# Performance work log

Measured on AMD Instinct MI355X. Metric: run time of the kernel, lower is better.

## Reference

```python
import jax, jax.numpy as jnp
import numpy as np

N_NODES = 100000
N_EDGES = 1600000
N_FEATS = 128
N_CLASSES = 40
K_HOPS = 3


def setup_inputs() -> dict:
    key = jax.random.key(0)
    k1, k2, k3, k4 = jax.random.split(key, 4)
    x = jax.random.normal(k1, (N_NODES, N_FEATS), dtype=jnp.float32)
    edge_index = jax.random.randint(k2, (2, N_EDGES), 0, N_NODES, dtype=jnp.int64)
    edge_weight = jax.random.uniform(k3, (N_EDGES,), dtype=jnp.float32)
    # Linear layer of SGConv (bias=False): [num_feats, num_classes]
    W = jax.random.normal(k4, (N_FEATS, N_CLASSES), dtype=jnp.float32) / np.sqrt(N_FEATS)
    return {"x": x, "edge_index": edge_index, "edge_weight": edge_weight, "W": W}


def reference(x, edge_index, edge_weight, W):
    # SGConv forward: gcn_norm (symmetric, no self-loops), K hops of
    # edge-weighted gather/scatter aggregation, then linear (lin_first=False).
    row, col = edge_index[0], edge_index[1]
    # symmetric normalization: deg from target-node scatter of edge weights
    deg = jax.ops.segment_sum(edge_weight, col, num_segments=N_NODES)
    deg_inv_sqrt = jnp.where(deg > 0, jax.lax.rsqrt(jnp.maximum(deg, 1e-30)), 0.0)
    norm = deg_inv_sqrt[row] * edge_weight * deg_inv_sqrt[col]  # [E]
    h = x
    for _ in range(K_HOPS):
        msgs = h[row] * norm[:, None]                 # [E, F] gather + scale
        h = jax.ops.segment_sum(msgs, col, num_segments=N_NODES)  # [N, F] scatter-add
    return h @ W  # [N, num_classes]
```

## Files before the change

### kernel.cpp

```cpp
#include <hip/hip_runtime.h>
#include <hip/hip_fp16.h>

namespace {
constexpr int NN = 100000;
constexpr int NE = 1600000;
constexpr int NF = 128;
constexpr int NC = 40;
constexpr int HP = 64;
constexpr int NB = (NN + 255) / 256;
constexpr int EB = (NE + 255) / 256;
constexpr float FIX = 1048576.0f;
constexpr int NPB = 51;
constexpr int HB  = (NN + NPB - 1) / NPB;
constexpr int TS  = 2048;
}

struct alignas(16) H8 { __half2 a, b, c, d; };

__device__ inline __half2 f2h2(float x, float y) {
    return __halves2half2(__float2half_rn(x), __float2half_rn(y));
}

__global__ __launch_bounds__(256, 2) void k_build(const int* __restrict__ col,
                                                  const float* __restrict__ w,
                                                  const float* __restrict__ x,
                                                  const float* __restrict__ W,
                                                  unsigned long long* __restrict__ dc,
                                                  unsigned char* __restrict__ rank,
                                                  __half* __restrict__ h0) {
    if (blockIdx.x < (unsigned)NB) {
        int n = blockIdx.x * 256 + threadIdx.x;
        if (n >= NN) return;
        const float4* xr = (const float4*)(x + (size_t)n * NF);
        const float4* W4 = (const float4*)W;
        float acc[NC];
#pragma unroll
        for (int j = 0; j < NC; ++j) acc[j] = 0.f;
        for (int k4 = 0; k4 < NF / 4; ++k4) {
            float4 xv = xr[k4];
#pragma unroll
            for (int kk = 0; kk < 4; ++kk) {
                float xk = (kk == 0) ? xv.x : (kk == 1) ? xv.y : (kk == 2) ? xv.z : xv.w;
                int k = k4 * 4 + kk;
#pragma unroll
                for (int j4 = 0; j4 < 10; ++j4) {
                    float4 wv = W4[k * 10 + j4];
                    acc[j4 * 4 + 0] += xk * wv.x;
                    acc[j4 * 4 + 1] += xk * wv.y;
                    acc[j4 * 4 + 2] += xk * wv.z;
                    acc[j4 * 4 + 3] += xk * wv.w;
                }
            }
        }
        H8* o = (H8*)(h0 + (size_t)n * HP);
#pragma unroll
        for (int g = 0; g < 5; ++g) {
            H8 v;
            v.a = f2h2(acc[g * 8 + 0], acc[g * 8 + 1]);
            v.b = f2h2(acc[g * 8 + 2], acc[g * 8 + 3]);
            v.c = f2h2(acc[g * 8 + 4], acc[g * 8 + 5]);
            v.d = f2h2(acc[g * 8 + 6], acc[g * 8 + 7]);
            o[g] = v;
        }
    } else {
        int e = (blockIdx.x - NB) * 256 + threadIdx.x;
        if (e >= NE) return;
        int c = col[e];
        unsigned long long q = (unsigned long long)(unsigned)(w[e] * FIX + 0.5f);
        unsigned long long old = atomicAdd(&dc[c], (1ull << 40) | q);
        rank[e] = (unsigned char)(old >> 40);
    }
}

__global__ __launch_bounds__(256) void k_scan1(const unsigned long long* __restrict__ dc,
                                               int* __restrict__ offs,
                                               int* __restrict__ bsum,
                                               float* __restrict__ dis) {
    __shared__ int s[256];
    int t = threadIdx.x, i = blockIdx.x * 256 + t;
    unsigned long long p = (i < NN) ? dc[i] : 0ull;
    int v = (int)(p >> 40);
    if (i < NN) {
        float d = (float)(p & ((1ull << 40) - 1)) * (1.0f / FIX);
        dis[i] = (d > 0.f) ? rsqrtf(d) : 0.f;
    }
    s[t] = v;
    __syncthreads();
    for (int off = 1; off < 256; off <<= 1) {
        int add = (t >= off) ? s[t - off] : 0;
        __syncthreads();
        s[t] += add;
        __syncthreads();
    }
    if (i < NN) offs[i] = s[t] - v;
    if (t == 255) bsum[blockIdx.x] = s[255];
}

__global__ __launch_bounds__(512) void k_scan2(int* __restrict__ bsum) {
    __shared__ int s[512];
    int t = threadIdx.x;
    int v = (t < NB) ? bsum[t] : 0;
    s[t] = v;
    __syncthreads();
    for (int off = 1; off < 512; off <<= 1) {
        int add = (t >= off) ? s[t - off] : 0;
        __syncthreads();
        s[t] += add;
        __syncthreads();
    }
    if (t < NB) bsum[t] = s[t] - v;
}

__global__ __launch_bounds__(256) void k_scatter(const int* __restrict__ row,
                                                 const int* __restrict__ col,
                                                 const float* __restrict__ w,
                                                 const float* __restrict__ dis,
                                                 const int* __restrict__ offs,
                                                 const int* __restrict__ bsum,
                                                 const unsigned char* __restrict__ rank,
                                                 int2* __restrict__ pair) {
    int e = blockIdx.x * 256 + threadIdx.x;
    if (e >= NE) return;
    int r = row[e], c = col[e];
    int p = offs[c] + bsum[c >> 8] + rank[e];
    unsigned long long v = (unsigned long long)(unsigned)r |
        ((unsigned long long)(unsigned)__float_as_int(dis[r] * w[e] * dis[c]) << 32);
    __builtin_nontemporal_store(v, (unsigned long long*)(pair + p));
}

template <bool FINAL>
__global__ __launch_bounds__(256) void k_hop(const int* __restrict__ offs,
                                             const int* __restrict__ bsum,
                                             const int2* __restrict__ pair,
                                             const __half* __restrict__ hin,
                                             __half* __restrict__ houth,
                                             float* __restrict__ houtf) {
    __shared__ int2 tile[TS];
    __shared__ int erange[2];
    int t = threadIdx.x;
    int g = t / 5;
    int n = blockIdx.x * NPB + g;
    bool active = (t < NPB * 5) && (n < NN);
    int vo = (t - g * 5) * 8;
    int s0 = 0, s1 = 0;
    if (active) {
        s0 = offs[n] + bsum[n >> 8];
        int np = n + 1;
        s1 = (np == NN) ? NE : (offs[np] + bsum[np >> 8]);
    }
    if (t == 0) {
        int n0 = blockIdx.x * NPB;
        erange[0] = offs[n0] + bsum[n0 >> 8];
        int nl = n0 + NPB;
        erange[1] = (nl >= NN) ? NE : (offs[nl] + bsum[nl >> 8]);
    }
    __syncthreads();
    int E0 = erange[0], E1 = erange[1];
    float acc[8];
#pragma unroll
    for (int j = 0; j < 8; ++j) acc[j] = 0.f;
    int i = s0;
    for (int t0 = E0; t0 < E1; t0 += TS) {
        int lim = min(t0 + TS, E1);
        int cnt = lim - t0;
        for (int j = t; j < cnt; j += 256) tile[j] = pair[t0 + j];
        __syncthreads();
        if (active) {
            int hi = min(s1, lim);
            for (; i + 2 <= hi; i += 2) {
                int2 p0 = tile[i - t0];
                int2 p1 = tile[i + 1 - t0];
                H8 m0 = *(const H8*)(hin + (size_t)p0.x * HP + vo);
                H8 m1 = *(const H8*)(hin + (size_t)p1.x * HP + vo);
                float w0 = __int_as_float(p0.y);
                float w1 = __int_as_float(p1.y);
                float2 f;
                f = __half22float2(m0.a); acc[0] += f.x * w0; acc[1] += f.y * w0;
                f = __half22float2(m0.b); acc[2] += f.x * w0; acc[3] += f.y * w0;
                f = __half22float2(m0.c); acc[4] += f.x * w0; acc[5] += f.y * w0;
                f = __half22float2(m0.d); acc[6] += f.x * w0; acc[7] += f.y * w0;
                f = __half22float2(m1.a); acc[0] += f.x * w1; acc[1] += f.y * w1;
                f = __half22float2(m1.b); acc[2] += f.x * w1; acc[3] += f.y * w1;
                f = __half22float2(m1.c); acc[4] += f.x * w1; acc[5] += f.y * w1;
                f = __half22float2(m1.d); acc[6] += f.x * w1; acc[7] += f.y * w1;
            }
            if (i < hi) {
                int2 p0 = tile[i - t0];
                H8 m0 = *(const H8*)(hin + (size_t)p0.x * HP + vo);
                float w0 = __int_as_float(p0.y);
                float2 f;
                f = __half22float2(m0.a); acc[0] += f.x * w0; acc[1] += f.y * w0;
                f = __half22float2(m0.b); acc[2] += f.x * w0; acc[3] += f.y * w0;
                f = __half22float2(m0.c); acc[4] += f.x * w0; acc[5] += f.y * w0;
                f = __half22float2(m0.d); acc[6] += f.x * w0; acc[7] += f.y * w0;
                ++i;
            }
        }
        __syncthreads();
    }
    if (active) {
        if (FINAL) {
            float* o = houtf + (size_t)n * NC + vo;
            float4 v0 = {acc[0], acc[1], acc[2], acc[3]};
            float4 v1 = {acc[4], acc[5], acc[6], acc[7]};
            *(float4*)(o) = v0;
            *(float4*)(o + 4) = v1;
        } else {
            H8 v;
            v.a = f2h2(acc[0], acc[1]);
            v.b = f2h2(acc[2], acc[3]);
            v.c = f2h2(acc[4], acc[5]);
            v.d = f2h2(acc[6], acc[7]);
            *(H8*)(houth + (size_t)n * HP + vo) = v;
        }
    }
}

extern "C" void kernel_launch(void* const* d_in, const int* in_sizes, int n_in,
                              void* d_out, int out_size, void* d_ws, size_t ws_size,
                              hipStream_t stream) {
    const float* x  = (const float*)d_in[0];
    const int*   ei = (const int*)d_in[1];
    const float* w  = (const float*)d_in[2];
    const float* W  = (const float*)d_in[3];
    const int* row = ei;
    const int* col = ei + NE;
    float* out = (float*)d_out;

    char* base = (char*)d_ws;
    __half* hb = (__half*)base;
    unsigned long long* dc = (unsigned long long*)base;
    float* dis = (float*)(base + (size_t)NN * 8);
    unsigned char* rank = (unsigned char*)(base + (size_t)NN * 12);
    char* p = base + (size_t)NN * HP * 2;
    int*  offs = (int*)p;   p += (size_t)(NN + 4) * 4;
    int*  bsum = (int*)p;   p += 512 * 4;
    int2* pair = (int2*)p;  p += (size_t)NE * 8;
    __half* ha = (__half*)p;

    hipMemsetAsync(dc, 0, (size_t)NN * 8, stream);
    k_build<<<NB + EB, 256, 0, stream>>>(col, w, x, W, dc, rank, ha);
    k_scan1<<<NB, 256, 0, stream>>>(dc, offs, bsum, dis);
    k_scan2<<<1, 512, 0, stream>>>(bsum);
    k_scatter<<<EB, 256, 0, stream>>>(row, col, w, dis, offs, bsum, rank, pair);

    k_hop<false><<<HB, 256, 0, stream>>>(offs, bsum, pair, ha, hb, nullptr);
    k_hop<false><<<HB, 256, 0, stream>>>(offs, bsum, pair, hb, ha, nullptr);
    k_hop<true ><<<HB, 256, 0, stream>>>(offs, bsum, pair, ha, nullptr, out);
}
```

Baseline: 328.6 us.

## Replace global-atomic CSR build with two-level bucket sort and rescaled normalization

Builds the CSR by first bucketing edges into fixed-capacity per-256-node staging regions with block-local histograms, then sorting within each bucket in shared memory. Degree accumulation moves from global 64-bit atomics into LDS. The symmetric normalization is also refactored: edge weights become w*dis[c]^2, the input is prescaled by dis and the output rescaled by sqrt(deg), which removes the random dis[row] gather. The hop inner loop is unrolled to 4 edges. This relies on a fixed bucket capacity (CAP=6144), which could overflow on skewed graphs. Algebraically it is equivalent except when deg is zero.

```diff
diff --git a/kernel.cpp b/kernel.cpp
--- a/kernel.cpp
+++ b/kernel.cpp
@@ -8,7 +8,9 @@
 constexpr int NC = 40;
 constexpr int HP = 64;
 constexpr int NB = (NN + 255) / 256;
-constexpr int EB = (NE + 255) / 256;
+constexpr int EPB = 4096;
+constexpr int EBK = (NE + EPB - 1) / EPB;
+constexpr int CAP = 6144;
 constexpr float FIX = 1048576.0f;
 constexpr int NPB = 51;
 constexpr int HB  = (NN + NPB - 1) / NPB;
@@ -21,16 +23,116 @@
     return __halves2half2(__float2half_rn(x), __float2half_rn(y));
 }
 
-__global__ __launch_bounds__(256, 2) void k_build(const int* __restrict__ col,
-                                                  const float* __restrict__ w,
+__global__ __launch_bounds__(256) void k_bucket(const int* __restrict__ col,
+                                                const int* __restrict__ row,
+                                                const float* __restrict__ w,
+                                                unsigned int* __restrict__ cursor,
+                                                int2* __restrict__ bstage) {
+    __shared__ unsigned int lhist[NB];
+    __shared__ unsigned int lbase[NB];
+    __shared__ unsigned int lrank[NB];
+    int t = threadIdx.x;
+    for (int i = t; i < NB; i += 256) { lhist[i] = 0u; lrank[i] = 0u; }
+    __syncthreads();
+    int e0 = blockIdx.x * EPB;
+    int e1 = min(e0 + EPB, NE);
+    for (int e = e0 + t; e < e1; e += 256)
+        atomicAdd(&lhist[col[e] >> 8], 1u);
+    __syncthreads();
+    for (int i = t; i < NB; i += 256) {
+        unsigned c = lhist[i];
+        lbase[i] = c ? atomicAdd(&cursor[i], c) : 0u;
+    }
+    __syncthreads();
+    for (int e = e0 + t; e < e1; e += 256) {
+        int c = col[e];
+        int b = c >> 8;
+        unsigned r = atomicAdd(&lrank[b], 1u);
+        int2 v;
+        v.x = (row[e] & 0x1FFFF) | ((c & 255) << 17);
+        v.y = __float_as_int(w[e]);
+        bstage[(size_t)b * CAP + lbase[b] + r] = v;
+    }
+}
+
+__global__ __launch_bounds__(512) void k_bscan(const unsigned int* __restrict__ cursor,
+                                               int* __restrict__ bbase,
+                                               int* __restrict__ offs) {
+    __shared__ int s[512];
+    int t = threadIdx.x;
+    int v = (t < NB) ? (int)cursor[t] : 0;
+    s[t] = v;
+    __syncthreads();
+    for (int off = 1; off < 512; off <<= 1) {
+        int add = (t >= off) ? s[t - off] : 0;
+        __syncthreads();
+        s[t] += add;
+        __syncthreads();
+    }
+    if (t < NB) bbase[t] = s[t] - v;
+    if (t == NB) bbase[NB] = s[NB - 1];
+    if (t == 0)  offs[NN] = NE;
+}
+
+__global__ __launch_bounds__(256) void k_sortgemm(const int2* __restrict__ bstage,
+                                                  const int* __restrict__ bbase,
                                                   const float* __restrict__ x,
                                                   const float* __restrict__ W,
-                                                  unsigned long long* __restrict__ dc,
-                                                  unsigned char* __restrict__ rank,
-                                                  __half* __restrict__ h0) {
-    if (blockIdx.x < (unsigned)NB) {
-        int n = blockIdx.x * 256 + threadIdx.x;
-        if (n >= NN) return;
+                                                  int* __restrict__ offs,
+                                                  float* __restrict__ invdis,
+                                                  int2* __restrict__ pair,
+                                                  __half* __restrict__ z0) {
+    __shared__ unsigned long long lpk[256];
+    __shared__ int ls[256];
+    __shared__ float ldis[256];
+    __shared__ unsigned int lrank[256];
+    int t = threadIdx.x;
+    int b = blockIdx.x;
+    int base = bbase[b];
+    int cnt  = bbase[b + 1] - base;
+    lpk[t] = 0ull;
+    lrank[t] = 0u;
+    __syncthreads();
+    const int2* bs = bstage + (size_t)b * CAP;
+    for (int j = t; j < cnt; j += 256) {
+        int2 s = bs[j];
+        int cl = (s.x >> 17) & 255;
+        unsigned long long q =
+            (unsigned long long)(unsigned)(__int_as_float(s.y) * FIX + 0.5f);
+        atomicAdd(&lpk[cl], (1ull << 40) | q);
+    }
+    __syncthreads();
+    int myc = (int)(lpk[t] >> 40);
+    float deg = (float)(lpk[t] & ((1ull << 40) - 1)) * (1.0f / FIX);
+    float dis = (deg > 0.f) ? rsqrtf(deg) : 0.f;
+    ldis[t] = dis;
+    ls[t] = myc;
+    __syncthreads();
+    for (int off = 1; off < 256; off <<= 1) {
+        int add = (t >= off) ? ls[t - off] : 0;
+        __syncthreads();
+        ls[t] += add;
+        __syncthreads();
+    }
+    int start = ls[t] - myc;
+    int n = b * 256 + t;
+    if (n < NN) {
+        offs[n] = base + start;
+        invdis[n] = sqrtf(fmaxf(deg, 0.f));
+    }
+    ls[t] = start;
+    __syncthreads();
+    for (int j = t; j < cnt; j += 256) {
+        int2 s = bs[j];
+        int cl = (s.x >> 17) & 255;
+        unsigned r = atomicAdd(&lrank[cl], 1u);
+        float d = ldis[cl];
+        int2 v;
+        v.x = s.x & 0x1FFFF;
+        v.y = __float_as_int(__int_as_float(s.y) * d * d);
+        pair[base + ls[cl] + r] = v;
+    }
+    if (n < NN) {
         const float4* xr = (const float4*)(x + (size_t)n * NF);
         const float4* W4 = (const float4*)W;
         float acc[NC];
@@ -52,89 +154,27 @@
                 }
             }
         }
-        H8* o = (H8*)(h0 + (size_t)n * HP);
+        float sc = ldis[t];
+        H8* o = (H8*)(z0 + (size_t)n * HP);
 #pragma unroll
         for (int g = 0; g < 5; ++g) {
             H8 v;
-            v.a = f2h2(acc[g * 8 + 0], acc[g * 8 + 1]);
-            v.b = f2h2(acc[g * 8 + 2], acc[g * 8 + 3]);
-            v.c = f2h2(acc[g * 8 + 4], acc[g * 8 + 5]);
-            v.d = f2h2(acc[g * 8 + 6], acc[g * 8 + 7]);
+            v.a = f2h2(acc[g * 8 + 0] * sc, acc[g * 8 + 1] * sc);
+            v.b = f2h2(acc[g * 8 + 2] * sc, acc[g * 8 + 3] * sc);
+            v.c = f2h2(acc[g * 8 + 4] * sc, acc[g * 8 + 5] * sc);
+            v.d = f2h2(acc[g * 8 + 6] * sc, acc[g * 8 + 7] * sc);
             o[g] = v;
         }
-    } else {
-        int e = (blockIdx.x - NB) * 256 + threadIdx.x;
-        if (e >= NE) return;
-        int c = col[e];
-        unsigned long long q = (unsigned long long)(unsigned)(w[e] * FIX + 0.5f);
-        unsigned long long old = atomicAdd(&dc[c], (1ull << 40) | q);
-        rank[e] = (unsigned char)(old >> 40);
-    }
-}
-
-__global__ __launch_bounds__(256) void k_scan1(const unsigned long long* __restrict__ dc,
-                                               int* __restrict__ offs,
-                                               int* __restrict__ bsum,
-                                               float* __restrict__ dis) {
-    __shared__ int s[256];
-    int t = threadIdx.x, i = blockIdx.x * 256 + t;
-    unsigned long long p = (i < NN) ? dc[i] : 0ull;
-    int v = (int)(p >> 40);
-    if (i < NN) {
-        float d = (float)(p & ((1ull << 40) - 1)) * (1.0f / FIX);
-        dis[i] = (d > 0.f) ? rsqrtf(d) : 0.f;
-    }
-    s[t] = v;
-    __syncthreads();
-    for (int off = 1; off < 256; off <<= 1) {
-        int add = (t >= off) ? s[t - off] : 0;
-        __syncthreads();
-        s[t] += add;
-        __syncthreads();
-    }
-    if (i < NN) offs[i] = s[t] - v;
-    if (t == 255) bsum[blockIdx.x] = s[255];
-}
-
-__global__ __launch_bounds__(512) void k_scan2(int* __restrict__ bsum) {
-    __shared__ int s[512];
-    int t = threadIdx.x;
-    int v = (t < NB) ? bsum[t] : 0;
-    s[t] = v;
-    __syncthreads();
-    for (int off = 1; off < 512; off <<= 1) {
-        int add = (t >= off) ? s[t - off] : 0;
-        __syncthreads();
-        s[t] += add;
-        __syncthreads();
-    }
-    if (t < NB) bsum[t] = s[t] - v;
-}
-
-__global__ __launch_bounds__(256) void k_scatter(const int* __restrict__ row,
-                                                 const int* __restrict__ col,
-                                                 const float* __restrict__ w,
-                                                 const float* __restrict__ dis,
-                                                 const int* __restrict__ offs,
-                                                 const int* __restrict__ bsum,
-                                                 const unsigned char* __restrict__ rank,
-                                                 int2* __restrict__ pair) {
-    int e = blockIdx.x * 256 + threadIdx.x;
-    if (e >= NE) return;
-    int r = row[e], c = col[e];
-    int p = offs[c] + bsum[c >> 8] + rank[e];
-    unsigned long long v = (unsigned long long)(unsigned)r |
-        ((unsigned long long)(unsigned)__float_as_int(dis[r] * w[e] * dis[c]) << 32);
-    __builtin_nontemporal_store(v, (unsigned long long*)(pair + p));
+    }
 }
 
 template <bool FINAL>
 __global__ __launch_bounds__(256) void k_hop(const int* __restrict__ offs,
-                                             const int* __restrict__ bsum,
                                              const int2* __restrict__ pair,
                                              const __half* __restrict__ hin,
                                              __half* __restrict__ houth,
-                                             float* __restrict__ houtf) {
+                                             float* __restrict__ houtf,
+                                             const float* __restrict__ invdis) {
     __shared__ int2 tile[TS];
     __shared__ int erange[2];
     int t = threadIdx.x;
@@ -144,15 +184,14 @@
     int vo = (t - g * 5) * 8;
     int s0 = 0, s1 = 0;
     if (active) {
-        s0 = offs[n] + bsum[n >> 8];
-        int np = n + 1;
-        s1 = (np == NN) ? NE : (offs[np] + bsum[np >> 8]);
+        s0 = offs[n];
+        s1 = offs[n + 1];
     }
     if (t == 0) {
         int n0 = blockIdx.x * NPB;
-        erange[0] = offs[n0] + bsum[n0 >> 8];
-        int nl = n0 + NPB;
-        erange[1] = (nl >= NN) ? NE : (offs[nl] + bsum[nl >> 8]);
+        int nl = min(n0 + NPB, NN);
+        erange[0] = offs[n0];
+        erange[1] = offs[nl];
     }
     __syncthreads();
     int E0 = erange[0], E1 = erange[1];
@@ -160,6 +199,11 @@
 #pragma unroll
     for (int j = 0; j < 8; ++j) acc[j] = 0.f;
     int i = s0;
+#define ACC8(m, wgt) { float2 f_;                                        \
+    f_ = __half22float2((m).a); acc[0] += f_.x * (wgt); acc[1] += f_.y * (wgt); \
+    f_ = __half22float2((m).b); acc[2] += f_.x * (wgt); acc[3] += f_.y * (wgt); \
+    f_ = __half22float2((m).c); acc[4] += f_.x * (wgt); acc[5] += f_.y * (wgt); \
+    f_ = __half22float2((m).d); acc[6] += f_.x * (wgt); acc[7] += f_.y * (wgt); }
     for (int t0 = E0; t0 < E1; t0 += TS) {
         int lim = min(t0 + TS, E1);
         int cnt = lim - t0;
@@ -167,42 +211,37 @@
         __syncthreads();
         if (active) {
             int hi = min(s1, lim);
-            for (; i + 2 <= hi; i += 2) {
+            for (; i + 4 <= hi; i += 4) {
                 int2 p0 = tile[i - t0];
                 int2 p1 = tile[i + 1 - t0];
+                int2 p2 = tile[i + 2 - t0];
+                int2 p3 = tile[i + 3 - t0];
                 H8 m0 = *(const H8*)(hin + (size_t)p0.x * HP + vo);
                 H8 m1 = *(const H8*)(hin + (size_t)p1.x * HP + vo);
+                H8 m2 = *(const H8*)(hin + (size_t)p2.x * HP + vo);
+                H8 m3 = *(const H8*)(hin + (size_t)p3.x * HP + vo);
                 float w0 = __int_as_float(p0.y);
                 float w1 = __int_as_float(p1.y);
-                float2 f;
-                f = __half22float2(m0.a); acc[0] += f.x * w0; acc[1] += f.y * w0;
-                f = __half22float2(m0.b); acc[2] += f.x * w0; acc[3] += f.y * w0;
-                f = __half22float2(m0.c); acc[4] += f.x * w0; acc[5] += f.y * w0;
-                f = __half22float2(m0.d); acc[6] += f.x * w0; acc[7] += f.y * w0;
-                f = __half22float2(m1.a); acc[0] += f.x * w1; acc[1] += f.y * w1;
-                f = __half22float2(m1.b); acc[2] += f.x * w1; acc[3] += f.y * w1;
-                f = __half22float2(m1.c); acc[4] += f.x * w1; acc[5] += f.y * w1;
-                f = __half22float2(m1.d); acc[6] += f.x * w1; acc[7] += f.y * w1;
+                float w2 = __int_as_float(p2.y);
+                float w3 = __int_as_float(p3.y);
+                ACC8(m0, w0) ACC8(m1, w1) ACC8(m2, w2) ACC8(m3, w3)
             }
-            if (i < hi) {
+            for (; i < hi; ++i) {
                 int2 p0 = tile[i - t0];
                 H8 m0 = *(const H8*)(hin + (size_t)p0.x * HP + vo);
                 float w0 = __int_as_float(p0.y);
-                float2 f;
-                f = __half22float2(m0.a); acc[0] += f.x * w0; acc[1] += f.y * w0;
-                f = __half22float2(m0.b); acc[2] += f.x * w0; acc[3] += f.y * w0;
-                f = __half22float2(m0.c); acc[4] += f.x * w0; acc[5] += f.y * w0;
-                f = __half22float2(m0.d); acc[6] += f.x * w0; acc[7] += f.y * w0;
-                ++i;
+                ACC8(m0, w0)
             }
         }
         __syncthreads();
     }
+#undef ACC8
     if (active) {
         if (FINAL) {
+            float sc = invdis[n];
             float* o = houtf + (size_t)n * NC + vo;
-            float4 v0 = {acc[0], acc[1], acc[2], acc[3]};
-            float4 v1 = {acc[4], acc[5], acc[6], acc[7]};
+            float4 v0 = {acc[0] * sc, acc[1] * sc, acc[2] * sc, acc[3] * sc};
+            float4 v1 = {acc[4] * sc, acc[5] * sc, acc[6] * sc, acc[7] * sc};
             *(float4*)(o) = v0;
             *(float4*)(o + 4) = v1;
         } else {
@@ -228,23 +267,22 @@
     float* out = (float*)d_out;
 
     char* base = (char*)d_ws;
-    __half* hb = (__half*)base;
-    unsigned long long* dc = (unsigned long long*)base;
-    float* dis = (float*)(base + (size_t)NN * 8);
-    unsigned char* rank = (unsigned char*)(base + (size_t)NN * 12);
-    char* p = base + (size_t)NN * HP * 2;
-    int*  offs = (int*)p;   p += (size_t)(NN + 4) * 4;
-    int*  bsum = (int*)p;   p += 512 * 4;
-    int2* pair = (int2*)p;  p += (size_t)NE * 8;
-    __half* ha = (__half*)p;
-
-    hipMemsetAsync(dc, 0, (size_t)NN * 8, stream);
-    k_build<<<NB + EB, 256, 0, stream>>>(col, w, x, W, dc, rank, ha);
-    k_scan1<<<NB, 256, 0, stream>>>(dc, offs, bsum, dis);
-    k_scan2<<<1, 512, 0, stream>>>(bsum);
-    k_scatter<<<EB, 256, 0, stream>>>(row, col, w, dis, offs, bsum, rank, pair);
-
-    k_hop<false><<<HB, 256, 0, stream>>>(offs, bsum, pair, ha, hb, nullptr);
-    k_hop<false><<<HB, 256, 0, stream>>>(offs, bsum, pair, hb, ha, nullptr);
-    k_hop<true ><<<HB, 256, 0, stream>>>(offs, bsum, pair, ha, nullptr, out);
-}
+    int2* bstage = (int2*)base;
+    __half* hb   = (__half*)base;
+    char* p = base + (size_t)NB * CAP * 8;
+    __half* ha = (__half*)p;        p += (size_t)NN * HP * 2;
+    int2* pair = (int2*)p;          p += (size_t)NE * 8;
+    int*  offs = (int*)p;           p += (size_t)(NN + 1) * 4;
+    int*  bbase = (int*)p;          p += (size_t)(NB + 1) * 4;
+    float* invdis = (float*)p;      p += (size_t)NN * 4;
+    unsigned int* cursor = (unsigned int*)p;
+
+    hipMemsetAsync(cursor, 0, (size_t)NB * 4, stream);
+    k_bucket<<<EBK, 256, 0, stream>>>(col, row, w, cursor, bstage);
+    k_bscan<<<1, 512, 0, stream>>>(cursor, bbase, offs);
+    k_sortgemm<<<NB, 256, 0, stream>>>(bstage, bbase, x, W, offs, invdis, pair, ha);
+
+    k_hop<false><<<HB, 256, 0, stream>>>(offs, pair, ha, hb, nullptr, nullptr);
+    k_hop<false><<<HB, 256, 0, stream>>>(offs, pair, hb, ha, nullptr, nullptr);
+    k_hop<true ><<<HB, 256, 0, stream>>>(offs, pair, ha, nullptr, out, invdis);
+}
```

Result: faster. 275.4 us (-16.2%).
